# Performance work log

Hardware: AMD Instinct MI355X
Metric: run time of the kernel (lower is better)

Reference implementation:

```python
import jax, jax.numpy as jnp
import numpy as np

TEMPERATURE = 0.07
EPS = 1e-12  # matches F.normalize eps clamp


def setup_inputs() -> dict:
    key = jax.random.key(0)
    k1, k2 = jax.random.split(key)
    B, S, D = 8, 512, 128
    return {
        "z_i": jax.random.normal(k1, (B, S, D), dtype=jnp.float32),
        "z_j": jax.random.normal(k2, (B, S, D), dtype=jnp.float32),
    }


def reference(z_i, z_j):
    D = z_i.shape[-1]
    zi = z_i.reshape(-1, D)  # [N, D]
    zj = z_j.reshape(-1, D)
    # cosine normalization (use_cosine_similarity=True)
    zi = zi / jnp.maximum(jnp.linalg.norm(zi, axis=1, keepdims=True), EPS)
    zj = zj / jnp.maximum(jnp.linalg.norm(zj, axis=1, keepdims=True), EPS)
    N = zi.shape[0]
    z = jnp.concatenate([zi, zj], axis=0)  # [2N, D]
    sim = (z @ z.T) / TEMPERATURE  # [2N, 2N]
    # denominator: logsumexp over all j != i (positives + negatives)
    diag = jnp.eye(2 * N, dtype=bool)
    lse = jax.nn.logsumexp(jnp.where(diag, -jnp.inf, sim), axis=1)  # [2N]
    # positive logit for row i is sim[i, (i+N) mod 2N] = <zi, zj>/T for both halves
    pos_half = jnp.sum(zi * zj, axis=1) / TEMPERATURE  # [N]
    pos = jnp.concatenate([pos_half, pos_half])  # [2N]
    return jnp.mean(-pos + lse)
```

## Files before the change

kernel.cpp:

```cpp
#include <hip/hip_runtime.h>
#include <stdint.h>


#define TOTAL   8192
#define NHALF   4096
#define DK      128
#define TEMP_INV 14.285714285714286f
#define SCALE    4.539816f

#define TILE    128
#define TILES   (TOTAL / TILE)
#define NBLK    (TILES * (TILES + 1) / 2)
#define WAVES   8

typedef short  bf16x8  __attribute__((ext_vector_type(8)));
typedef float  floatx4 __attribute__((ext_vector_type(4)));

#if __has_builtin(__builtin_amdgcn_exp2f)
#define EXP2(x) __builtin_amdgcn_exp2f(x)
#else
#define EXP2(x) exp2f(x)
#endif

__device__ __forceinline__ uint32_t f2bf(float f) {
  uint32_t u = __float_as_uint(f);
  return (u + 0x7fffu + ((u >> 16) & 1u)) >> 16;
}
__device__ __forceinline__ uint32_t pack2bf(float lo, float hi) {
  return f2bf(lo) | (f2bf(hi) << 16);
}

__global__ __launch_bounds__(256) void ntx_norm(
    const float* __restrict__ zi, const float* __restrict__ zj,
    uint32_t* __restrict__ zn,
    float* __restrict__ pos)
{
  const int t = threadIdx.x;
  const int wave = t >> 6, lane = t & 63;
  const int i = blockIdx.x * 4 + wave;

  const float2 vi = *(const float2*)(zi + (size_t)i * DK + lane * 2);
  const float2 vj = *(const float2*)(zj + (size_t)i * DK + lane * 2);
  float ssi = vi.x * vi.x + vi.y * vi.y;
  float ssj = vj.x * vj.x + vj.y * vj.y;
  float dij = vi.x * vj.x + vi.y * vj.y;
#pragma unroll
  for (int m = 1; m <= 32; m <<= 1) {
    ssi += __shfl_xor(ssi, m, 64);
    ssj += __shfl_xor(ssj, m, 64);
    dij += __shfl_xor(dij, m, 64);
  }
  const float invi = 1.0f / fmaxf(sqrtf(ssi), 1e-12f);
  const float invj = 1.0f / fmaxf(sqrtf(ssj), 1e-12f);

  zn[(size_t)i * 64 + lane] =
      pack2bf(vi.x * invi * SCALE, vi.y * invi * SCALE);
  zn[(size_t)(i + NHALF) * 64 + lane] =
      pack2bf(vj.x * invj * SCALE, vj.y * invj * SCALE);
  if (lane == 0) pos[i] = dij * invi * invj * TEMP_INV;
}

__global__ __launch_bounds__(512, 8) void ntx_gemm(
    const uint16_t* __restrict__ z,
    float* __restrict__ scratch)
{
  __shared__ uint4 lb4[TILE * 17];
  __shared__ float colacc[WAVES][TILE];

  int I = 0, rem = (int)blockIdx.x, span = TILES;
  while (rem >= span) { rem -= span; --span; ++I; }
  const int J = I + rem;
  const bool isdiag = (I == J);

  const int t = threadIdx.x;
  const int w = t >> 6, lane = t & 63;
  const int q = lane >> 4, c = lane & 15;
  const int i0 = I * TILE;
  const int j0 = J * TILE;
  const int rowbase = i0 + w * 16;

  bf16x8 afrag[4];
  {
    const uint16_t* ap = z + (size_t)(rowbase + c) * DK + q * 8;
#pragma unroll
    for (int kk = 0; kk < 4; ++kk)
      afrag[kk] = *(const bf16x8*)(ap + kk * 32);
  }

  {
    const int r0 = t >> 4, ch = t & 15;
#pragma unroll
    for (int p = 0; p < 4; ++p) {
      const int r = r0 + p * 32;
      lb4[r * 17 + ch] = *(const uint4*)(z + (size_t)(j0 + r) * DK + ch * 8);
    }
  }
  __syncthreads();

  float runsum[4] = {0.0f, 0.0f, 0.0f, 0.0f};

#pragma unroll
  for (int jt = 0; jt < TILE / 16; ++jt) {
    const int jc = j0 + jt * 16;
    bf16x8 bfrag[4];
#pragma unroll
    for (int kk = 0; kk < 4; ++kk)
      bfrag[kk] = *(const bf16x8*)&lb4[(jt * 16 + c) * 17 + kk * 4 + q];

    floatx4 acc = {0.0f, 0.0f, 0.0f, 0.0f};
#pragma unroll
    for (int kk = 0; kk < 4; ++kk)
      acc = __builtin_amdgcn_mfma_f32_16x16x32_bf16(afrag[kk], bfrag[kk],
                                                    acc, 0, 0, 0);
    if (isdiag && jc == rowbase) {
#pragma unroll
      for (int r = 0; r < 4; ++r) {
        float e = EXP2(acc[r]);
        runsum[r] += (q * 4 + r == c) ? 0.0f : e;
      }
    } else {
      float colv = 0.0f;
#pragma unroll
      for (int r = 0; r < 4; ++r) {
        float e = EXP2(acc[r]);
        runsum[r] += e;
        colv += e;
      }
      if (!isdiag) {
        colv += __shfl_xor(colv, 16, 64);
        colv += __shfl_xor(colv, 32, 64);
        if (lane < 16) colacc[w][jt * 16 + lane] = colv;
      }
    }
  }

  float* sblk = scratch + (size_t)blockIdx.x * 256;
#pragma unroll
  for (int r = 0; r < 4; ++r) {
    float v = runsum[r];
    v += __shfl_xor(v, 1, 64);
    v += __shfl_xor(v, 2, 64);
    v += __shfl_xor(v, 4, 64);
    v += __shfl_xor(v, 8, 64);
    if (c == 0) sblk[w * 16 + q * 4 + r] = v;
  }

  __syncthreads();
  if (!isdiag && t < TILE) {
    float s = 0.0f;
#pragma unroll
    for (int ww = 0; ww < WAVES; ++ww) s += colacc[ww][t];
    sblk[128 + t] = s;
  }
}

__global__ __launch_bounds__(256) void ntx_redu(
    const float* __restrict__ scratch, float* __restrict__ lpart)
{
  __shared__ float sbuf[128];
  __shared__ float red[2];

  const int I = (int)blockIdx.x;
  const int o = (int)threadIdx.x & 127;
  const int half = (int)threadIdx.x >> 7;

  float S = 0.0f;
  if (half == 0) {
    int id = I * TILES - (I * (I - 1)) / 2;
#pragma unroll 8
    for (int Jt = I; Jt < TILES; ++Jt, ++id)
      S += scratch[(size_t)id * 256 + o];
  } else {
    int idc = I;
#pragma unroll 8
    for (int Ip = 0; Ip < I; ++Ip) {
      S += scratch[(size_t)idc * 256 + 128 + o];
      idc += TILES - 1 - Ip;
    }
  }
  if (half) sbuf[o] = S;
  __syncthreads();
  if (!half) {
    float v = __logf(S + sbuf[o]);
#pragma unroll
    for (int m = 1; m <= 32; m <<= 1) v += __shfl_xor(v, m, 64);
    if ((o & 63) == 0) red[o >> 6] = v;
  }
  __syncthreads();
  if (threadIdx.x == 0) lpart[I] = red[0] + red[1];
}

__global__ __launch_bounds__(256) void ntx_final(
    const float* __restrict__ lpart, const float* __restrict__ pos,
    float* __restrict__ out)
{
  const int t = threadIdx.x;
  float acc = (t < TILES) ? lpart[t] : 0.0f;
  for (int r = t; r < NHALF; r += 256) acc -= 2.0f * pos[r];
#pragma unroll
  for (int m = 1; m <= 32; m <<= 1) acc += __shfl_xor(acc, m, 64);
  __shared__ float red[4];
  if ((t & 63) == 0) red[t >> 6] = acc;
  __syncthreads();
  if (t == 0) out[0] = (red[0] + red[1] + red[2] + red[3]) / (float)TOTAL;
}

extern "C" void kernel_launch(void* const* d_in, const int* in_sizes, int n_in,
                              void* d_out, int out_size, void* d_ws,
                              size_t ws_size, hipStream_t stream) {
  const float* zi = (const float*)d_in[0];
  const float* zj = (const float*)d_in[1];
  float* out = (float*)d_out;

  char* ws = (char*)d_ws;
  uint16_t* zn      = (uint16_t*)ws;
  float*    scratch = (float*)(ws + (size_t)TOTAL * DK * 2);
  float*    lpart   = (float*)(ws + (size_t)TOTAL * DK * 2
                               + (size_t)NBLK * 256 * 4);
  float*    pos     = (float*)(ws + (size_t)TOTAL * DK * 2
                               + (size_t)NBLK * 256 * 4 + 256);

  ntx_norm<<<dim3(NHALF / 4), dim3(256), 0, stream>>>(zi, zj, (uint32_t*)zn,
                                                      pos);
  ntx_gemm<<<dim3(NBLK), dim3(512), 0, stream>>>(zn, scratch);
  ntx_redu<<<dim3(TILES), dim3(256), 0, stream>>>(scratch, lpart);
  ntx_final<<<dim3(1), dim3(256), 0, stream>>>(lpart, pos, out);
}
```

Measured before the change: 90.41 us.

## Retile symmetric GEMM waves into 32x64 subtiles to reuse B fragments

Each wave now computes a 32-row by 64-column subtile instead of 16 rows by all 128 columns. Every B fragment loaded from LDS then feeds two MFMAs, which halves LDS reads per MFMA and gives two independent accumulator chains. Row and column partial sums are combined across waves through shared memory before being written out. This costs more A-fragment registers and adds an extra reduction step through LDS.

```diff
diff --git a/kernel.cpp b/kernel.cpp
--- a/kernel.cpp
+++ b/kernel.cpp
@@ -65,7 +65,8 @@
     float* __restrict__ scratch)
 {
   __shared__ uint4 lb4[TILE * 17];
-  __shared__ float colacc[WAVES][TILE];
+  __shared__ float rowacc[WAVES][32];
+  __shared__ float colacc[WAVES][64];
 
   int I = 0, rem = (int)blockIdx.x, span = TILES;
   while (rem >= span) { rem -= span; --span; ++I; }
@@ -75,16 +76,19 @@
   const int t = threadIdx.x;
   const int w = t >> 6, lane = t & 63;
   const int q = lane >> 4, c = lane & 15;
+  const int rg = w >> 1, cg = w & 1;
   const int i0 = I * TILE;
   const int j0 = J * TILE;
-  const int rowbase = i0 + w * 16;
-
-  bf16x8 afrag[4];
-  {
-    const uint16_t* ap = z + (size_t)(rowbase + c) * DK + q * 8;
+  const int rowbase = i0 + rg * 32;
+  const int colbase = j0 + cg * 64;
+
+  bf16x8 afrag[2][4];
+#pragma unroll
+  for (int s = 0; s < 2; ++s) {
+    const uint16_t* ap = z + (size_t)(rowbase + s * 16 + c) * DK + q * 8;
 #pragma unroll
     for (int kk = 0; kk < 4; ++kk)
-      afrag[kk] = *(const bf16x8*)(ap + kk * 32);
+      afrag[s][kk] = *(const bf16x8*)(ap + kk * 32);
   }
 
   {
@@ -97,60 +101,92 @@
   }
   __syncthreads();
 
-  float runsum[4] = {0.0f, 0.0f, 0.0f, 0.0f};
-
-#pragma unroll
-  for (int jt = 0; jt < TILE / 16; ++jt) {
-    const int jc = j0 + jt * 16;
-    bf16x8 bfrag[4];
-#pragma unroll
-    for (int kk = 0; kk < 4; ++kk)
-      bfrag[kk] = *(const bf16x8*)&lb4[(jt * 16 + c) * 17 + kk * 4 + q];
-
-    floatx4 acc = {0.0f, 0.0f, 0.0f, 0.0f};
-#pragma unroll
-    for (int kk = 0; kk < 4; ++kk)
-      acc = __builtin_amdgcn_mfma_f32_16x16x32_bf16(afrag[kk], bfrag[kk],
-                                                    acc, 0, 0, 0);
+  float runsum[2][4];
+#pragma unroll
+  for (int s = 0; s < 2; ++s)
+#pragma unroll
+    for (int r = 0; r < 4; ++r) runsum[s][r] = 0.0f;
+
+#pragma unroll
+  for (int jt = 0; jt < 4; ++jt) {
+    const int jc = colbase + jt * 16;
+    const int ldsrow = (cg * 64 + jt * 16 + c) * 17;
+
+    floatx4 acc0 = {0.0f, 0.0f, 0.0f, 0.0f};
+    floatx4 acc1 = {0.0f, 0.0f, 0.0f, 0.0f};
+#pragma unroll
+    for (int kh = 0; kh < 2; ++kh) {
+      const bf16x8 b0 = *(const bf16x8*)&lb4[ldsrow + (kh * 2 + 0) * 4 + q];
+      const bf16x8 b1 = *(const bf16x8*)&lb4[ldsrow + (kh * 2 + 1) * 4 + q];
+      acc0 = __builtin_amdgcn_mfma_f32_16x16x32_bf16(afrag[0][kh * 2 + 0], b0,
+                                                     acc0, 0, 0, 0);
+      acc0 = __builtin_amdgcn_mfma_f32_16x16x32_bf16(afrag[0][kh * 2 + 1], b1,
+                                                     acc0, 0, 0, 0);
+      acc1 = __builtin_amdgcn_mfma_f32_16x16x32_bf16(afrag[1][kh * 2 + 0], b0,
+                                                     acc1, 0, 0, 0);
+      acc1 = __builtin_amdgcn_mfma_f32_16x16x32_bf16(afrag[1][kh * 2 + 1], b1,
+                                                     acc1, 0, 0, 0);
+    }
+
+    float colv = 0.0f;
     if (isdiag && jc == rowbase) {
 #pragma unroll
       for (int r = 0; r < 4; ++r) {
-        float e = EXP2(acc[r]);
-        runsum[r] += (q * 4 + r == c) ? 0.0f : e;
+        float e = EXP2(acc0[r]);
+        runsum[0][r] += (q * 4 + r == c) ? 0.0f : e;
       }
     } else {
-      float colv = 0.0f;
-#pragma unroll
-      for (int r = 0; r < 4; ++r) {
-        float e = EXP2(acc[r]);
-        runsum[r] += e;
+#pragma unroll
+      for (int r = 0; r < 4; ++r) {
+        float e = EXP2(acc0[r]);
+        runsum[0][r] += e;
         colv += e;
       }
-      if (!isdiag) {
-        colv += __shfl_xor(colv, 16, 64);
-        colv += __shfl_xor(colv, 32, 64);
-        if (lane < 16) colacc[w][jt * 16 + lane] = colv;
-      }
-    }
-  }
-
+    }
+    if (isdiag && jc == rowbase + 16) {
+#pragma unroll
+      for (int r = 0; r < 4; ++r) {
+        float e = EXP2(acc1[r]);
+        runsum[1][r] += (q * 4 + r == c) ? 0.0f : e;
+      }
+    } else {
+#pragma unroll
+      for (int r = 0; r < 4; ++r) {
+        float e = EXP2(acc1[r]);
+        runsum[1][r] += e;
+        colv += e;
+      }
+    }
+
+    if (!isdiag) {
+      colv += __shfl_xor(colv, 16, 64);
+      colv += __shfl_xor(colv, 32, 64);
+      if (lane < 16) colacc[w][jt * 16 + lane] = colv;
+    }
+  }
+
+#pragma unroll
+  for (int s = 0; s < 2; ++s)
+#pragma unroll
+    for (int r = 0; r < 4; ++r) {
+      float v = runsum[s][r];
+      v += __shfl_xor(v, 1, 64);
+      v += __shfl_xor(v, 2, 64);
+      v += __shfl_xor(v, 4, 64);
+      v += __shfl_xor(v, 8, 64);
+      if (c == 0) rowacc[w][s * 16 + q * 4 + r] = v;
+    }
+
+  __syncthreads();
   float* sblk = scratch + (size_t)blockIdx.x * 256;
-#pragma unroll
-  for (int r = 0; r < 4; ++r) {
-    float v = runsum[r];
-    v += __shfl_xor(v, 1, 64);
-    v += __shfl_xor(v, 2, 64);
-    v += __shfl_xor(v, 4, 64);
-    v += __shfl_xor(v, 8, 64);
-    if (c == 0) sblk[w * 16 + q * 4 + r] = v;
-  }
-
-  __syncthreads();
-  if (!isdiag && t < TILE) {
-    float s = 0.0f;
-#pragma unroll
-    for (int ww = 0; ww < WAVES; ++ww) s += colacc[ww][t];
-    sblk[128 + t] = s;
+  if (t < TILE) {
+    const int rrg = t >> 5, ro = t & 31;
+    sblk[t] = rowacc[2 * rrg][ro] + rowacc[2 * rrg + 1][ro];
+    if (!isdiag) {
+      const int ccg = t >> 6, co = t & 63;
+      sblk[128 + t] = colacc[ccg][co] + colacc[ccg + 2][co] +
+                      colacc[ccg + 4][co] + colacc[ccg + 6][co];
+    }
   }
 }
 
```

Measured after the change: 106.9 us. 1.18x slower.
